# Kernel optimization log

Hardware: AMD Instinct MI355X
Metric: run time of the kernel (lower is better)

Reference implementation:

```python
import jax, jax.numpy as jnp
import numpy as np

H = 8
D = 512
DK = D // H
B = 16
N = 8192


def setup_inputs() -> dict:
    key = jax.random.key(0)
    k1, k2, k3, k4 = jax.random.split(key, 4)
    x = jax.random.normal(k1, (B, N, D), dtype=jnp.float32)
    W_k = jax.random.normal(k2, (D, D), dtype=jnp.float32) * (1.0 / np.sqrt(D))
    W_g = jax.random.normal(k3, (D, D), dtype=jnp.float32) * (1.0 / np.sqrt(D))
    query = jax.random.normal(k4, (H, 1, DK), dtype=jnp.float32)
    return {"x": x, "W_k": W_k, "W_g": W_g, "query": query}


def reference(x, W_k, W_g, query):
    b, n, d = x.shape
    # nn.Linear: y = x @ W.T  (no bias)
    K = (x @ W_k.T).reshape(b, n, H, DK).transpose(0, 2, 1, 3)  # (b,h,n,dk)
    G = (x @ W_g.T).reshape(b, n, H, DK).transpose(0, 2, 1, 3)  # (b,h,n,dk)
    xh = x.reshape(b, n, H, DK).transpose(0, 2, 1, 3)           # (b,h,n,dk)
    gated = jnp.tanh(K) * jax.nn.sigmoid(G)                     # (b,h,n,dk)
    # single-query attention: scores (b,h,1,n)
    scores = jnp.einsum('hmd,bhnd->bhmn', query, gated)
    attn = jax.nn.softmax(scores, axis=-1)
    out = jnp.einsum('bhmn,bhnd->bhmd', attn, xh)               # (b,h,1,dk)
    out = out.transpose(0, 2, 1, 3).reshape(b, 1, H * DK)
    return out.squeeze()  # (b, d)
```

## Files before the change

### kernel.cpp

```cpp
#include <hip/hip_runtime.h>
#include <hip/hip_bf16.h>

#define H_ 8
#define D_ 512
#define DK_ 64
#define B_ 16
#define N_ 8192
#define M_ (B_ * N_)

typedef __attribute__((ext_vector_type(8))) short short8;
typedef __attribute__((ext_vector_type(4))) float floatx4;

__device__ __forceinline__ void glds16(const void* g, void* l) {
    __builtin_amdgcn_global_load_lds((const __attribute__((address_space(1))) void*)g,
                                     (__attribute__((address_space(3))) void*)l,
                                     16, 0, 0);
}

__device__ __forceinline__ unsigned short f2bf(float f) {
    unsigned u = __float_as_uint(f);
    return (unsigned short)((u + 0x7fffu + ((u >> 16) & 1u)) >> 16);
}

__device__ __forceinline__ unsigned cvt_pk(float lo, float hi) {
    unsigned r;
    asm("v_cvt_pk_bf16_f32 %0, %1, %2" : "=v"(r) : "v"(lo), "v"(hi));
    return r;
}

__device__ __forceinline__ short8 pack_bf8(float4 lo, float4 hi) {
    union { unsigned u[4]; short8 s; } tmp;
    tmp.u[0] = cvt_pk(lo.x, lo.y);
    tmp.u[1] = cvt_pk(lo.z, lo.w);
    tmp.u[2] = cvt_pk(hi.x, hi.y);
    tmp.u[3] = cvt_pk(hi.z, hi.w);
    return tmp.s;
}

__global__ __launch_bounds__(256) void cvt_kernel(const float* __restrict__ src,
                                                  unsigned short* __restrict__ dst, int n4) {
    int i = blockIdx.x * blockDim.x + threadIdx.x;
    int stride = gridDim.x * blockDim.x;
    for (; i < n4; i += stride) {
        float4 v = ((const float4*)src)[i];
        ushort4 o;
        o.x = f2bf(v.x); o.y = f2bf(v.y); o.z = f2bf(v.z); o.w = f2bf(v.w);
        ((ushort4*)dst)[i] = o;
    }
}

__global__ __launch_bounds__(256, 2) void gemm_score_kernel(
    const float* __restrict__ x,
    const unsigned short* __restrict__ wkb,
    const unsigned short* __restrict__ wgb,
    const float* __restrict__ query,
    float* __restrict__ s_buf)
{
    __shared__ __attribute__((aligned(16))) unsigned short lds_a[128 * 64];
    __shared__ __attribute__((aligned(16))) unsigned short lds_k[128 * 64];
    __shared__ __attribute__((aligned(16))) unsigned short lds_g[128 * 64];

    const int t = threadIdx.x;
    const int lane = t & 63;
    const int wave = t >> 6;
    const int wm = wave >> 1, wn = wave & 1;
    const int fr = lane & 15;
    const int q4 = lane >> 4;
    const int sw = fr & 7;

    const int g = blockIdx.x;
    const int xcd = g & 7;
    const int s = g >> 3;
    const int jt = s & 3;
    const int mt = ((s >> 2) << 3) | xcd;
    const int jc = jt * 128;
    const int m0 = mt * 128;

    const int ar = t >> 3;
    const int ac = t & 7;
    const float* pA = x + (size_t)(m0 + ar) * 512 + ac * 8;
    const int awoff = ar * 64 + (ac ^ (ar & 7)) * 8;

    int boff[4];
#pragma unroll
    for (int i = 0; i < 4; ++i) {
        int p = i * 256 + t;
        int r = p >> 3;
        int c = (p & 7) ^ (r & 7);
        boff[i] = (jc + r) * 512 + c * 8;
    }

    floatx4 acc_k[4][4], acc_g[4][4];
#pragma unroll
    for (int i = 0; i < 4; ++i)
#pragma unroll
        for (int j = 0; j < 4; ++j) { acc_k[i][j] = (floatx4)0.f; acc_g[i][j] = (floatx4)0.f; }

    for (int k0 = 0; k0 < 512; k0 += 64) {
#pragma unroll
        for (int i = 0; i < 4; ++i) {
            glds16(wkb + boff[i] + k0, lds_k + (size_t)(i * 256 + t) * 8);
            glds16(wgb + boff[i] + k0, lds_g + (size_t)(i * 256 + t) * 8);
        }
        float4 av[8];
#pragma unroll
        for (int it = 0; it < 4; ++it) {
            const float* p = pA + (size_t)it * (32 * 512) + k0;
            av[it * 2]     = *(const float4*)(p);
            av[it * 2 + 1] = *(const float4*)(p + 4);
        }
#pragma unroll
        for (int it = 0; it < 4; ++it)
            *(short8*)&lds_a[it * (32 * 64) + awoff] = pack_bf8(av[it * 2], av[it * 2 + 1]);
        __syncthreads();

#pragma unroll
        for (int kc = 0; kc < 2; ++kc) {
            short8 a[4], bk[4], bg[4];
#pragma unroll
            for (int mi = 0; mi < 4; ++mi) {
                int off = (wm * 64 + mi * 16 + fr) * 64 + (q4 ^ sw) * 8;
                a[mi] = *(const short8*)&lds_a[off ^ (kc * 32)];
            }
#pragma unroll
            for (int ni = 0; ni < 4; ++ni) {
                int off = (wn * 64 + ni * 16 + fr) * 64 + (q4 ^ sw) * 8;
                bk[ni] = *(const short8*)&lds_k[off ^ (kc * 32)];
                bg[ni] = *(const short8*)&lds_g[off ^ (kc * 32)];
            }
#pragma unroll
            for (int mi = 0; mi < 4; ++mi)
#pragma unroll
                for (int ni = 0; ni < 4; ++ni) {
                    acc_k[mi][ni] = __builtin_amdgcn_mfma_f32_16x16x32_bf16(a[mi], bk[ni], acc_k[mi][ni], 0, 0, 0);
                    acc_g[mi][ni] = __builtin_amdgcn_mfma_f32_16x16x32_bf16(a[mi], bg[ni], acc_g[mi][ni], 0, 0, 0);
                }
        }
        __syncthreads();
    }

    const int h = jt * 2 + wn;
    float qv[4];
#pragma unroll
    for (int ni = 0; ni < 4; ++ni) qv[ni] = query[h * 64 + ni * 16 + fr];

#pragma unroll
    for (int mi = 0; mi < 4; ++mi) {
#pragma unroll
        for (int r = 0; r < 4; ++r) {
            float v = 0.f;
#pragma unroll
            for (int ni = 0; ni < 4; ++ni) {
                float kv = acc_k[mi][ni][r];
                float gv = acc_g[mi][ni][r];
                float e2k = fminf(__expf(2.f * kv), 1e18f);
                float eg  = fminf(__expf(gv),      1e18f);
                float num = (e2k - 1.f) * eg;
                float den = (e2k + 1.f) * (eg + 1.f);
                v += qv[ni] * num * __builtin_amdgcn_rcpf(den);
            }
            v += __shfl_xor(v, 1);
            v += __shfl_xor(v, 2);
            v += __shfl_xor(v, 4);
            v += __shfl_xor(v, 8);
            if (fr == 0) {
                int mg = m0 + wm * 64 + mi * 16 + q4 * 4 + r;
                int b = mg >> 13, n = mg & 8191;
                s_buf[((size_t)(b * 8 + h) << 13) + n] = v;
            }
        }
    }
}

__global__ __launch_bounds__(256) void stats_kernel(const float* __restrict__ s_buf,
                                                    float* __restrict__ mb, float* __restrict__ lb) {
    const int bh = blockIdx.x;
    const float4* s4 = (const float4*)(s_buf + ((size_t)bh << 13));
    const int t = threadIdx.x;
    float4 vv[8];
    float mx = -3.0e38f;
#pragma unroll
    for (int i = 0; i < 8; ++i) {
        float4 v = s4[t + i * 256];
        vv[i] = v;
        mx = fmaxf(mx, fmaxf(fmaxf(v.x, v.y), fmaxf(v.z, v.w)));
    }
#pragma unroll
    for (int m = 32; m > 0; m >>= 1) mx = fmaxf(mx, __shfl_xor(mx, m));
    __shared__ float red[8];
    if ((t & 63) == 0) red[t >> 6] = mx;
    __syncthreads();
    mx = fmaxf(fmaxf(red[0], red[1]), fmaxf(red[2], red[3]));
    float sum = 0.f;
#pragma unroll
    for (int i = 0; i < 8; ++i) {
        float4 v = vv[i];
        sum += __expf(v.x - mx) + __expf(v.y - mx) + __expf(v.z - mx) + __expf(v.w - mx);
    }
#pragma unroll
    for (int m = 32; m > 0; m >>= 1) sum += __shfl_xor(sum, m);
    if ((t & 63) == 0) red[4 + (t >> 6)] = sum;
    __syncthreads();
    if (t == 0) { mb[bh] = mx; lb[bh] = 1.f / (red[4] + red[5] + red[6] + red[7]); }
}

__global__ __launch_bounds__(256) void out_kernel(
    const float* __restrict__ x, const float* __restrict__ s_buf,
    const float* __restrict__ mb, const float* __restrict__ lb,
    float* __restrict__ out) {
    const int b = blockIdx.x >> 6;
    const int chunk = blockIdx.x & 63;
    const int n0 = chunk * 128;
    const int t = threadIdx.x;
    __shared__ float w[8 * 128];
    __shared__ float red[3 * 512];
    for (int i = t; i < 1024; i += 256) {
        int hh = i >> 7, nn = i & 127;
        int bh = b * 8 + hh;
        w[i] = __expf(s_buf[((size_t)bh << 13) + n0 + nn] - mb[bh]) * lb[bh];
    }
    __syncthreads();
    const int rg = t >> 6;
    const int d0 = (t & 63) * 8;
    const float* wh = w + ((d0 >> 6) << 7);
    const float* xb = x + (((size_t)(b * 8192 + n0)) << 9) + d0;
    float acc[8] = {0.f, 0.f, 0.f, 0.f, 0.f, 0.f, 0.f, 0.f};
    for (int i = 0; i < 32; i += 2) {
        const int n1 = rg + i * 4;
        const int n2 = n1 + 4;
        const float4* r1p = (const float4*)(xb + ((size_t)n1 << 9));
        const float4* r2p = (const float4*)(xb + ((size_t)n2 << 9));
        float4 a0 = r1p[0];
        float4 a1 = r1p[1];
        float4 b0 = r2p[0];
        float4 b1 = r2p[1];
        float w1 = wh[n1];
        float w2 = wh[n2];
        acc[0] += w1 * a0.x; acc[1] += w1 * a0.y; acc[2] += w1 * a0.z; acc[3] += w1 * a0.w;
        acc[4] += w1 * a1.x; acc[5] += w1 * a1.y; acc[6] += w1 * a1.z; acc[7] += w1 * a1.w;
        acc[0] += w2 * b0.x; acc[1] += w2 * b0.y; acc[2] += w2 * b0.z; acc[3] += w2 * b0.w;
        acc[4] += w2 * b1.x; acc[5] += w2 * b1.y; acc[6] += w2 * b1.z; acc[7] += w2 * b1.w;
    }
    if (rg != 0) {
#pragma unroll
        for (int j = 0; j < 8; ++j) red[(rg - 1) * 512 + (t & 63) * 8 + j] = acc[j];
    }
    __syncthreads();
    if (rg == 0) {
#pragma unroll
        for (int j = 0; j < 8; ++j) {
            float v = acc[j] + red[(t & 63) * 8 + j] + red[512 + (t & 63) * 8 + j]
                    + red[1024 + (t & 63) * 8 + j];
            atomicAdd(&out[b * 512 + d0 + j], v);
        }
    }
}

extern "C" void kernel_launch(void* const* d_in, const int* in_sizes, int n_in,
                              void* d_out, int out_size, void* d_ws, size_t ws_size,
                              hipStream_t stream) {
    const float* x  = (const float*)d_in[0];
    const float* Wk = (const float*)d_in[1];
    const float* Wg = (const float*)d_in[2];
    const float* q  = (const float*)d_in[3];
    float* out = (float*)d_out;

    char* ws = (char*)d_ws;
    unsigned short* wkb = (unsigned short*)ws;
    unsigned short* wgb = (unsigned short*)(ws + 524288ull);
    float* s_buf = (float*)(ws + 1048576ull);
    float* mb = (float*)(ws + 5242880ull);
    float* lb = (float*)(ws + 5243392ull);

    hipMemsetAsync(d_out, 0, 512 * B_ * sizeof(float), stream);

    hipLaunchKernelGGL(cvt_kernel, dim3(256), dim3(256), 0, stream, Wk, wkb, (D_ * D_) / 4);
    hipLaunchKernelGGL(cvt_kernel, dim3(256), dim3(256), 0, stream, Wg, wgb, (D_ * D_) / 4);
    hipLaunchKernelGGL(gemm_score_kernel, dim3(4096), dim3(256), 0, stream, x, wkb, wgb, q, s_buf);
    hipLaunchKernelGGL(stats_kernel, dim3(128), dim3(256), 0, stream, s_buf, mb, lb);
    hipLaunchKernelGGL(out_kernel, dim3(1024), dim3(256), 0, stream, x, s_buf, mb, lb, out);
}
```

Baseline: 550.0 us.

## Pre-convert x to bf16 and stream it via direct-to-LDS loads in GEMM

Adds a fused conversion kernel that turns x and both weight matrices into bf16 in workspace. A new GEMM variant then loads the A tile with global_load_lds, double-buffered. The aim is to halve the bytes the GEMM reads for x across its repeated column tiles and to overlap A loads with MFMA work. The cost is an extra full pass over x, a read plus a bf16 write. The path only runs when the workspace is large enough; otherwise the old kernel is used.

```diff
diff --git a/kernel.cpp b/kernel.cpp
--- a/kernel.cpp
+++ b/kernel.cpp
@@ -35,6 +35,27 @@
     tmp.u[2] = cvt_pk(hi.x, hi.y);
     tmp.u[3] = cvt_pk(hi.z, hi.w);
     return tmp.s;
+}
+
+#define NX4_ ((M_ * D_) / 4)
+#define NW4_ ((D_ * D_) / 4)
+__global__ __launch_bounds__(256) void cvt3_kernel(
+    const float* __restrict__ x, const float* __restrict__ wk, const float* __restrict__ wg,
+    unsigned short* __restrict__ xb, unsigned short* __restrict__ wkb, unsigned short* __restrict__ wgb) {
+    int i = blockIdx.x * blockDim.x + threadIdx.x;
+    const int stride = gridDim.x * blockDim.x;
+    const int total = NX4_ + 2 * NW4_;
+    for (; i < total; i += stride) {
+        const float4* src;
+        ushort4* dst;
+        if (i < NX4_)              { src = (const float4*)x  + i;             dst = (ushort4*)xb  + i; }
+        else if (i < NX4_ + NW4_)  { src = (const float4*)wk + (i - NX4_);    dst = (ushort4*)wkb + (i - NX4_); }
+        else                       { src = (const float4*)wg + (i - NX4_ - NW4_); dst = (ushort4*)wgb + (i - NX4_ - NW4_); }
+        float4 v = *src;
+        ushort4 o;
+        o.x = f2bf(v.x); o.y = f2bf(v.y); o.z = f2bf(v.z); o.w = f2bf(v.w);
+        *dst = o;
+    }
 }
 
 __global__ __launch_bounds__(256) void cvt_kernel(const float* __restrict__ src,
@@ -50,6 +71,138 @@
 }
 
 __global__ __launch_bounds__(256, 2) void gemm_score_kernel(
+    const unsigned short* __restrict__ xb,
+    const unsigned short* __restrict__ wkb,
+    const unsigned short* __restrict__ wgb,
+    const float* __restrict__ query,
+    float* __restrict__ s_buf)
+{
+    __shared__ __attribute__((aligned(16))) unsigned short lds_a[2][128 * 64];
+    __shared__ __attribute__((aligned(16))) unsigned short lds_k[128 * 64];
+    __shared__ __attribute__((aligned(16))) unsigned short lds_g[128 * 64];
+
+    const int t = threadIdx.x;
+    const int lane = t & 63;
+    const int wave = t >> 6;
+    const int wm = wave >> 1, wn = wave & 1;
+    const int fr = lane & 15;
+    const int q4 = lane >> 4;
+    const int sw = fr & 7;
+
+    const int g = blockIdx.x;
+    const int xcd = g & 7;
+    const int s = g >> 3;
+    const int jt = s & 3;
+    const int mt = ((s >> 2) << 3) | xcd;
+    const int jc = jt * 128;
+    const int m0 = mt * 128;
+
+    size_t aoff[4];
+    int boff[4];
+#pragma unroll
+    for (int i = 0; i < 4; ++i) {
+        int p = i * 256 + t;
+        int r = p >> 3;
+        int c = (p & 7) ^ (r & 7);
+        aoff[i] = (size_t)(m0 + r) * 512 + c * 8;
+        boff[i] = (jc + r) * 512 + c * 8;
+    }
+
+    floatx4 acc_k[4][4], acc_g[4][4];
+#pragma unroll
+    for (int i = 0; i < 4; ++i)
+#pragma unroll
+        for (int j = 0; j < 4; ++j) { acc_k[i][j] = (floatx4)0.f; acc_g[i][j] = (floatx4)0.f; }
+
+#pragma unroll
+    for (int i = 0; i < 4; ++i)
+        glds16(xb + aoff[i], &lds_a[0][(size_t)(i * 256 + t) * 8]);
+#pragma unroll
+    for (int i = 0; i < 4; ++i) {
+        glds16(wkb + boff[i], lds_k + (size_t)(i * 256 + t) * 8);
+        glds16(wgb + boff[i], lds_g + (size_t)(i * 256 + t) * 8);
+    }
+    __syncthreads();
+
+    for (int kt = 0; kt < 8; ++kt) {
+        const int cur = kt & 1;
+        const unsigned short* la = lds_a[cur];
+        const int k1 = (kt + 1) * 64;
+
+        if (kt < 7) {
+#pragma unroll
+            for (int i = 0; i < 4; ++i)
+                glds16(xb + aoff[i] + k1, &lds_a[cur ^ 1][(size_t)(i * 256 + t) * 8]);
+        }
+
+#pragma unroll
+        for (int kc = 0; kc < 2; ++kc) {
+            short8 a[4], bk[4], bg[4];
+#pragma unroll
+            for (int mi = 0; mi < 4; ++mi) {
+                int off = (wm * 64 + mi * 16 + fr) * 64 + (q4 ^ sw) * 8;
+                a[mi] = *(const short8*)&la[off ^ (kc * 32)];
+            }
+#pragma unroll
+            for (int ni = 0; ni < 4; ++ni) {
+                int off = (wn * 64 + ni * 16 + fr) * 64 + (q4 ^ sw) * 8;
+                bk[ni] = *(const short8*)&lds_k[off ^ (kc * 32)];
+                bg[ni] = *(const short8*)&lds_g[off ^ (kc * 32)];
+            }
+#pragma unroll
+            for (int mi = 0; mi < 4; ++mi)
+#pragma unroll
+                for (int ni = 0; ni < 4; ++ni) {
+                    acc_k[mi][ni] = __builtin_amdgcn_mfma_f32_16x16x32_bf16(a[mi], bk[ni], acc_k[mi][ni], 0, 0, 0);
+                    acc_g[mi][ni] = __builtin_amdgcn_mfma_f32_16x16x32_bf16(a[mi], bg[ni], acc_g[mi][ni], 0, 0, 0);
+                }
+        }
+
+        if (kt < 7) {
+            __syncthreads();
+#pragma unroll
+            for (int i = 0; i < 4; ++i) {
+                glds16(wkb + boff[i] + k1, lds_k + (size_t)(i * 256 + t) * 8);
+                glds16(wgb + boff[i] + k1, lds_g + (size_t)(i * 256 + t) * 8);
+            }
+            __syncthreads();
+        }
+    }
+
+    const int h = jt * 2 + wn;
+    float qv[4];
+#pragma unroll
+    for (int ni = 0; ni < 4; ++ni) qv[ni] = query[h * 64 + ni * 16 + fr];
+
+#pragma unroll
+    for (int mi = 0; mi < 4; ++mi) {
+#pragma unroll
+        for (int r = 0; r < 4; ++r) {
+            float v = 0.f;
+#pragma unroll
+            for (int ni = 0; ni < 4; ++ni) {
+                float kv = acc_k[mi][ni][r];
+                float gv = acc_g[mi][ni][r];
+                float e2k = fminf(__expf(2.f * kv), 1e18f);
+                float eg  = fminf(__expf(gv),      1e18f);
+                float num = (e2k - 1.f) * eg;
+                float den = (e2k + 1.f) * (eg + 1.f);
+                v += qv[ni] * num * __builtin_amdgcn_rcpf(den);
+            }
+            v += __shfl_xor(v, 1);
+            v += __shfl_xor(v, 2);
+            v += __shfl_xor(v, 4);
+            v += __shfl_xor(v, 8);
+            if (fr == 0) {
+                int mg = m0 + wm * 64 + mi * 16 + q4 * 4 + r;
+                int b = mg >> 13, n = mg & 8191;
+                s_buf[((size_t)(b * 8 + h) << 13) + n] = v;
+            }
+        }
+    }
+}
+
+__global__ __launch_bounds__(256, 2) void gemm_score_kernel_fb(
     const float* __restrict__ x,
     const unsigned short* __restrict__ wkb,
     const unsigned short* __restrict__ wgb,
@@ -271,12 +424,20 @@
     float* s_buf = (float*)(ws + 1048576ull);
     float* mb = (float*)(ws + 5242880ull);
     float* lb = (float*)(ws + 5243392ull);
+    unsigned short* xb = (unsigned short*)(ws + (8ull << 20));
+
+    const bool big_ws = ws_size >= (136ull << 20);
 
     hipMemsetAsync(d_out, 0, 512 * B_ * sizeof(float), stream);
 
-    hipLaunchKernelGGL(cvt_kernel, dim3(256), dim3(256), 0, stream, Wk, wkb, (D_ * D_) / 4);
-    hipLaunchKernelGGL(cvt_kernel, dim3(256), dim3(256), 0, stream, Wg, wgb, (D_ * D_) / 4);
-    hipLaunchKernelGGL(gemm_score_kernel, dim3(4096), dim3(256), 0, stream, x, wkb, wgb, q, s_buf);
+    if (big_ws) {
+        hipLaunchKernelGGL(cvt3_kernel, dim3(2048), dim3(256), 0, stream, x, Wk, Wg, xb, wkb, wgb);
+        hipLaunchKernelGGL(gemm_score_kernel, dim3(4096), dim3(256), 0, stream, xb, wkb, wgb, q, s_buf);
+    } else {
+        hipLaunchKernelGGL(cvt_kernel, dim3(256), dim3(256), 0, stream, Wk, wkb, (D_ * D_) / 4);
+        hipLaunchKernelGGL(cvt_kernel, dim3(256), dim3(256), 0, stream, Wg, wgb, (D_ * D_) / 4);
+        hipLaunchKernelGGL(gemm_score_kernel_fb, dim3(4096), dim3(256), 0, stream, x, wkb, wgb, q, s_buf);
+    }
     hipLaunchKernelGGL(stats_kernel, dim3(128), dim3(256), 0, stream, s_buf, mb, lb);
     hipLaunchKernelGGL(out_kernel, dim3(1024), dim3(256), 0, stream, x, s_buf, mb, lb, out);
 }
```

New measurement: 594.7 us. 8.1% more time.
